# Performance work log

Measured on AMD Instinct MI355X. Metric: run time of the kernel, lower is better.

Reference implementation:

```python
import jax, jax.numpy as jnp
import numpy as np

B, N, D = 8, 4096, 256
H = 8
DH = D // H          # 32 per-head dim
M = 256              # number of random features
DEPTH = 4
HID = 4 * D          # mlp hidden
EPS = 1e-6


def layernorm(x, g, b):
    mu = jnp.mean(x, axis=-1, keepdims=True)
    var = jnp.mean(jnp.square(x - mu), axis=-1, keepdims=True)
    return (x - mu) * jax.lax.rsqrt(var + EPS) * g + b


def _phi(t, proj, is_query):
    # t: (B,H,N,DH), proj: (M,DH) -> (B,H,N,M) nonnegative softmax-kernel features
    nrm = DH ** -0.25
    td = t * nrm
    u = jnp.einsum('bhnd,md->bhnm', td, proj)
    diag = 0.5 * jnp.sum(td * td, axis=-1, keepdims=True)
    if is_query:
        mx = jnp.max(u, axis=-1, keepdims=True)
    else:
        mx = jnp.max(u, axis=(-2, -1), keepdims=True)
    return (jnp.exp(u - diag - mx) + 1e-4) / jnp.sqrt(jnp.asarray(M, t.dtype))


def performer_attn(h, Wqkv, Wproj, bproj, proj):
    # h: (B,N,D)
    qkv = h @ Wqkv                                   # (B,N,3D)
    q, k, v = jnp.split(qkv, 3, axis=-1)
    to_heads = lambda t: t.reshape(B, N, H, DH).transpose(0, 2, 1, 3)
    q, k, v = to_heads(q), to_heads(k), to_heads(v)  # (B,H,N,DH)
    qp = _phi(q, proj, True)                         # (B,H,N,M)
    kp = _phi(k, proj, False)                        # (B,H,N,M)
    kv = jnp.einsum('bhnm,bhnd->bhmd', kp, v)        # (B,H,M,DH) linear-time context
    z = 1.0 / (jnp.einsum('bhnm,bhm->bhn', qp, kp.sum(axis=2)) + 1e-6)
    out = jnp.einsum('bhnm,bhmd->bhnd', qp, kv) * z[..., None]
    out = out.transpose(0, 2, 1, 3).reshape(B, N, D)
    return out @ Wproj + bproj


def mlp(h, W1, b1, W2, b2):
    return jax.nn.gelu(h @ W1 + b1, approximate=False) @ W2 + b2


def setup_inputs() -> dict:
    key = jax.random.key(0)
    ks = jax.random.split(key, 10)
    inp = {
        'x': jax.random.normal(ks[0], (B, N, D), jnp.float32),
        'pos_emb': 0.02 * jax.random.normal(ks[1], (N, D), jnp.float32),
        'g1n': jnp.ones((D,), jnp.float32),
        'b1n': jnp.zeros((D,), jnp.float32),
        'g2n': jnp.ones((D,), jnp.float32),
        'b2n': jnp.zeros((D,), jnp.float32),
        'Wqkv': 0.02 * jax.random.normal(ks[2], (DEPTH, D, 3 * D), jnp.float32),
        'Wproj': 0.02 * jax.random.normal(ks[3], (DEPTH, D, D), jnp.float32),
        'bproj': jnp.zeros((DEPTH, D), jnp.float32),
        'W1': 0.02 * jax.random.normal(ks[4], (DEPTH, D, HID), jnp.float32),
        'b1m': jnp.zeros((DEPTH, HID), jnp.float32),
        'W2': 0.02 * jax.random.normal(ks[5], (DEPTH, HID, D), jnp.float32),
        'b2m': jnp.zeros((DEPTH, D), jnp.float32),
        'proj_mat': jax.random.normal(ks[6], (DEPTH, M, DH), jnp.float32),
    }
    return inp


def reference(x, pos_emb, g1n, b1n, g2n, b2n, Wqkv, Wproj, bproj, W1, b1m, W2, b2m, proj_mat):
    h = x + pos_emb[None]
    for l in range(DEPTH):  # small fixed depth
        h = h + performer_attn(layernorm(h, g1n, b1n), Wqkv[l], Wproj[l], bproj[l], proj_mat[l])
        h = h + mlp(layernorm(h, g2n, b2n), W1[l], b1m[l], W2[l], b2m[l])
    return h
```

## Files before the change

kernel.cpp:

```cpp
#include <hip/hip_runtime.h>
#include <hip/hip_bf16.h>
#include <math.h>

#define B 8
#define N 4096
#define D 256
#define H 8
#define DH 32
#define M 256
#define DEPTH 4
#define HID 1024
#define NRM 0.4204482076268573f

typedef __attribute__((ext_vector_type(8))) short short8;
typedef __attribute__((ext_vector_type(4))) float f32x4;

static __device__ __forceinline__ unsigned short f2bf(float f) {
    __hip_bfloat16 h = __float2bfloat16(f);
    return __builtin_bit_cast(unsigned short, h);
}
static __device__ __forceinline__ float bfu2f(unsigned short u) {
    unsigned int x = ((unsigned int)u) << 16;
    return __builtin_bit_cast(float, x);
}

__global__ void add_pos_kernel(const float* __restrict__ x, const float* __restrict__ pos,
                               float* __restrict__ h) {
    int i = blockIdx.x * 256 + threadIdx.x;
    int nd = i % (N * D);
    h[i] = x[i] + pos[nd];
}

__global__ void projbf_kernel(const float* __restrict__ in, unsigned short* __restrict__ out) {
    int i = blockIdx.x * 256 + threadIdx.x;
    out[i] = f2bf(in[i]);
}

__global__ __launch_bounds__(256) void wtrans_kernel(const float* __restrict__ in,
                                                     unsigned short* __restrict__ out,
                                                     int Kd, int Nd, int slim) {
    __shared__ float tl[32][33];
    int n0 = blockIdx.x * 32, k0 = blockIdx.y * 32;
    int t = threadIdx.x;
    int kk = t >> 3, c4 = (t & 7) * 4;
    float4 v = *reinterpret_cast<const float4*>(&in[(size_t)(k0 + kk) * Nd + n0 + c4]);
    tl[kk][c4 + 0] = v.x; tl[kk][c4 + 1] = v.y; tl[kk][c4 + 2] = v.z; tl[kk][c4 + 3] = v.w;
    __syncthreads();
    int nn = t >> 3, k4 = (t & 7) * 4;
    float sc = (n0 + nn < slim) ? NRM : 1.0f;
    ushort4 o;
    o.x = f2bf(tl[k4 + 0][nn] * sc); o.y = f2bf(tl[k4 + 1][nn] * sc);
    o.z = f2bf(tl[k4 + 2][nn] * sc); o.w = f2bf(tl[k4 + 3][nn] * sc);
    *reinterpret_cast<ushort4*>(&out[(size_t)(n0 + nn) * Kd + k0 + k4]) = o;
}

__global__ __launch_bounds__(256) void ln_kernel(const float* __restrict__ in,
                                                 const float* __restrict__ g,
                                                 const float* __restrict__ bb,
                                                 unsigned short* __restrict__ out) {
    int wave = threadIdx.x >> 6, lane = threadIdx.x & 63;
    long row = (long)blockIdx.x * 4 + wave;
    float4 v = reinterpret_cast<const float4*>(in + row * D)[lane];
    float s = v.x + v.y + v.z + v.w;
#pragma unroll
    for (int o = 32; o >= 1; o >>= 1) s += __shfl_xor(s, o);
    float mu = s * (1.0f / D);
    float d0 = v.x - mu, d1 = v.y - mu, d2 = v.z - mu, d3 = v.w - mu;
    float ss = d0 * d0 + d1 * d1 + d2 * d2 + d3 * d3;
#pragma unroll
    for (int o = 32; o >= 1; o >>= 1) ss += __shfl_xor(ss, o);
    float inv = rsqrtf(ss * (1.0f / D) + 1e-6f);
    float4 gv = reinterpret_cast<const float4*>(g)[lane];
    float4 bv = reinterpret_cast<const float4*>(bb)[lane];
    ushort4 o4;
    o4.x = f2bf(d0 * inv * gv.x + bv.x);
    o4.y = f2bf(d1 * inv * gv.y + bv.y);
    o4.z = f2bf(d2 * inv * gv.z + bv.z);
    o4.w = f2bf(d3 * inv * gv.w + bv.w);
    *reinterpret_cast<ushort4*>(&out[row * D + lane * 4]) = o4;
}

template <bool BIAS, bool GELU_ACT, bool RESID, bool OUT16>
__global__ __launch_bounds__(256) void mgemm_kernel(const unsigned short* __restrict__ A,
                                                    const unsigned short* __restrict__ Bt,
                                                    const float* __restrict__ bias,
                                                    float* __restrict__ C,
                                                    unsigned short* __restrict__ O16,
                                                    int K, int Nc) {
    __shared__ short Als[128][40];
    __shared__ short Bls[128][40];
    int t = threadIdx.x;
    int l = t & 63, w = t >> 6;
    int wr = w >> 1, wc = w & 1;
    int nwg = gridDim.x * gridDim.y;
    int bid = blockIdx.y * gridDim.x + blockIdx.x;
    int lgid = (bid & 7) * (nwg >> 3) + (bid >> 3);
    int bx = lgid % gridDim.x;
    int by = lgid / gridDim.x;
    long m0 = (long)by * 128;
    int n0 = bx * 128;
    int lr = l & 15;
    int lg = l >> 4;
    int kp8 = lg * 8;
    int srow = t >> 2, skoff = (t & 3) * 8;

    const unsigned short* Ap0 = &A[(size_t)(m0 + srow) * K + skoff];
    const unsigned short* Ap1 = Ap0 + (size_t)64 * K;
    const unsigned short* Bp0 = &Bt[(size_t)(n0 + srow) * K + skoff];
    const unsigned short* Bp1 = Bp0 + (size_t)64 * K;

    short8 ra0 = *reinterpret_cast<const short8*>(Ap0);
    short8 ra1 = *reinterpret_cast<const short8*>(Ap1);
    short8 rb0 = *reinterpret_cast<const short8*>(Bp0);
    short8 rb1 = *reinterpret_cast<const short8*>(Bp1);

    f32x4 acc[4][4];
#pragma unroll
    for (int i = 0; i < 4; i++)
#pragma unroll
        for (int j = 0; j < 4; j++) acc[i][j] = (f32x4){0.f, 0.f, 0.f, 0.f};

    for (int k0 = 0; k0 < K; k0 += 32) {
        *reinterpret_cast<short8*>(&Als[srow][skoff]) = ra0;
        *reinterpret_cast<short8*>(&Als[srow + 64][skoff]) = ra1;
        *reinterpret_cast<short8*>(&Bls[srow][skoff]) = rb0;
        *reinterpret_cast<short8*>(&Bls[srow + 64][skoff]) = rb1;
        __syncthreads();
        if (k0 + 32 < K) {
            ra0 = *reinterpret_cast<const short8*>(Ap0 + k0 + 32);
            ra1 = *reinterpret_cast<const short8*>(Ap1 + k0 + 32);
            rb0 = *reinterpret_cast<const short8*>(Bp0 + k0 + 32);
            rb1 = *reinterpret_cast<const short8*>(Bp1 + k0 + 32);
        }
        short8 a[4], b[4];
#pragma unroll
        for (int i = 0; i < 4; i++)
            a[i] = *reinterpret_cast<const short8*>(&Als[wr * 64 + i * 16 + lr][kp8]);
#pragma unroll
        for (int j = 0; j < 4; j++)
            b[j] = *reinterpret_cast<const short8*>(&Bls[wc * 64 + j * 16 + lr][kp8]);
#pragma unroll
        for (int i = 0; i < 4; i++)
#pragma unroll
            for (int j = 0; j < 4; j++)
                acc[i][j] = __builtin_amdgcn_mfma_f32_16x16x32_bf16(b[j], a[i], acc[i][j], 0, 0, 0);
        __syncthreads();
    }

    float4 bias4[4];
    if (BIAS) {
#pragma unroll
        for (int j = 0; j < 4; j++)
            bias4[j] = *reinterpret_cast<const float4*>(&bias[n0 + wc * 64 + j * 16 + lg * 4]);
    }
#pragma unroll
    for (int i = 0; i < 4; i++) {
        long grow = m0 + wr * 64 + i * 16 + lr;
#pragma unroll
        for (int j = 0; j < 4; j++) {
            int gcol = n0 + wc * 64 + j * 16 + lg * 4;
            f32x4 v = acc[i][j];
            if (BIAS) {
                v[0] += bias4[j].x; v[1] += bias4[j].y; v[2] += bias4[j].z; v[3] += bias4[j].w;
            }
            if (GELU_ACT) {
#pragma unroll
                for (int r = 0; r < 4; r++)
                    v[r] = 0.5f * v[r] * (1.0f + erff(v[r] * 0.70710678118654752f));
            }
            if (OUT16) {
                short4 o;
                o.x = (short)f2bf(v[0]); o.y = (short)f2bf(v[1]);
                o.z = (short)f2bf(v[2]); o.w = (short)f2bf(v[3]);
                *reinterpret_cast<short4*>(&O16[grow * Nc + gcol]) = o;
            } else if (RESID) {
                float4 c0 = *reinterpret_cast<const float4*>(&C[grow * Nc + gcol]);
                c0.x += v[0]; c0.y += v[1]; c0.z += v[2]; c0.w += v[3];
                *reinterpret_cast<float4*>(&C[grow * Nc + gcol]) = c0;
            } else {
                float4 c0 = {v[0], v[1], v[2], v[3]};
                *reinterpret_cast<float4*>(&C[grow * Nc + gcol]) = c0;
            }
        }
    }
}

#define KV_P 16
#define KV_ROWS (N / KV_P)
#define PSZ 8484
__global__ __launch_bounds__(256) void kv_kernel(const unsigned short* __restrict__ qkv16,
                                                 const unsigned short* __restrict__ projbf,
                                                 float* __restrict__ kvp) {
    __shared__ __align__(16) unsigned short kp_s[256][64];
    __shared__ __align__(16) unsigned short vT_s[32][66];
    __shared__ float red[4];
    __shared__ float asumred[4][256];
    __shared__ float vred[256][4];
    int t = threadIdx.x;
    int l = t & 63, w = t >> 6;
    int lr = l & 15, lg = l >> 4;
    int bh = blockIdx.x, b = bh >> 3, h = bh & 7;
    int n0 = blockIdx.y * KV_ROWS;
    int rsw = (lr & 7) << 3;

    f32x4 kvacc[4][2];
#pragma unroll
    for (int mf = 0; mf < 4; mf++)
#pragma unroll
        for (int dd = 0; dd < 2; dd++) kvacc[mf][dd] = (f32x4){0.f, 0.f, 0.f, 0.f};
    float asum_p[16];
#pragma unroll
    for (int f = 0; f < 16; f++) asum_p[f] = 0.f;
    float4 vs4 = {0.f, 0.f, 0.f, 0.f};
    float Lm = -1e30f;

    for (int c = 0; c < KV_ROWS / 64; c++) {
        size_t kbase = ((size_t)(b * N) + n0 + c * 64 + w * 16 + lr) * 768 + 256 + h * 32 + lg * 8;
        short8 aq = *reinterpret_cast<const short8*>(qkv16 + kbase);
        float sq = 0.f;
#pragma unroll
        for (int e = 0; e < 8; e++) {
            float xx = bfu2f((unsigned short)aq[e]);
            sq += xx * xx;
        }
        sq += __shfl_xor(sq, 16);
        sq += __shfl_xor(sq, 32);
        f32x4 ua[16];
#pragma unroll
        for (int f = 0; f < 16; f++) {
            short8 bq = *reinterpret_cast<const short8*>(projbf + (f * 16 + lr) * 32 + lg * 8);
            ua[f] = __builtin_amdgcn_mfma_f32_16x16x32_bf16(aq, bq, (f32x4){0.f, 0.f, 0.f, 0.f}, 0, 0, 0);
        }
        float cm = -1e30f;
#pragma unroll
        for (int f = 0; f < 16; f++)
#pragma unroll
            for (int r = 0; r < 4; r++) cm = fmaxf(cm, ua[f][r]);
#pragma unroll
        for (int o = 1; o < 64; o <<= 1) cm = fmaxf(cm, __shfl_xor(cm, o));
        if (l == 0) red[w] = cm;
        __syncthreads();
        float bm = fmaxf(fmaxf(red[0], red[1]), fmaxf(red[2], red[3]));
        if (bm > Lm) {
            float sc = __expf(Lm - bm);
#pragma unroll
            for (int mf = 0; mf < 4; mf++)
#pragma unroll
                for (int dd = 0; dd < 2; dd++) {
                    kvacc[mf][dd][0] *= sc; kvacc[mf][dd][1] *= sc;
                    kvacc[mf][dd][2] *= sc; kvacc[mf][dd][3] *= sc;
                }
#pragma unroll
            for (int f = 0; f < 16; f++) asum_p[f] *= sc;
            Lm = bm;
        }
        float dgr[4];
#pragma unroll
        for (int r = 0; r < 4; r++) dgr[r] = 0.5f * __shfl(sq, lg * 4 + r);
        int cbase = (w * 16 + lg * 4) ^ rsw;
#pragma unroll
        for (int f = 0; f < 16; f++) {
            float p0 = __expf(ua[f][0] - dgr[0] - Lm);
            float p1 = __expf(ua[f][1] - dgr[1] - Lm);
            float p2 = __expf(ua[f][2] - dgr[2] - Lm);
            float p3 = __expf(ua[f][3] - dgr[3] - Lm);
            asum_p[f] += p0 + p1 + p2 + p3;
            short4 o;
            o.x = (short)f2bf(p0); o.y = (short)f2bf(p1);
            o.z = (short)f2bf(p2); o.w = (short)f2bf(p3);
            *reinterpret_cast<short4*>(&kp_s[f * 16 + lr][cbase]) = o;
        }
#pragma unroll
        for (int ii = 0; ii < 2; ii++) {
            int idx = t + ii * 256;
            int nn = idx >> 3, dz = (idx & 7) * 4;
            const unsigned short* vp =
                qkv16 + ((size_t)(b * N) + n0 + c * 64 + nn) * 768 + 512 + h * 32 + dz;
            short4 vv = *reinterpret_cast<const short4*>(vp);
            float v0 = bfu2f((unsigned short)vv.x), v1 = bfu2f((unsigned short)vv.y);
            float v2 = bfu2f((unsigned short)vv.z), v3 = bfu2f((unsigned short)vv.w);
            vs4.x += v0; vs4.y += v1; vs4.z += v2; vs4.w += v3;
            vT_s[dz + 0][nn] = (unsigned short)vv.x; vT_s[dz + 1][nn] = (unsigned short)vv.y;
            vT_s[dz + 2][nn] = (unsigned short)vv.z; vT_s[dz + 3][nn] = (unsigned short)vv.w;
        }
        __syncthreads();
#pragma unroll
        for (int ks = 0; ks < 2; ks++) {
            short8 bv0 = *reinterpret_cast<const short8*>(&vT_s[lr][ks * 32 + lg * 8]);
            short8 bv1 = *reinterpret_cast<const short8*>(&vT_s[16 + lr][ks * 32 + lg * 8]);
#pragma unroll
            for (int mf = 0; mf < 4; mf++) {
                short8 am = *reinterpret_cast<const short8*>(
                    &kp_s[w * 64 + mf * 16 + lr][(ks * 32 + lg * 8) ^ rsw]);
                kvacc[mf][0] = __builtin_amdgcn_mfma_f32_16x16x32_bf16(am, bv0, kvacc[mf][0], 0, 0, 0);
                kvacc[mf][1] = __builtin_amdgcn_mfma_f32_16x16x32_bf16(am, bv1, kvacc[mf][1], 0, 0, 0);
            }
        }
    }
#pragma unroll
    for (int f = 0; f < 16; f++) {
        asum_p[f] += __shfl_xor(asum_p[f], 16);
        asum_p[f] += __shfl_xor(asum_p[f], 32);
    }
    if (l < 16) {
#pragma unroll
        for (int f = 0; f < 16; f++) asumred[w][f * 16 + l] = asum_p[f];
    }
    vred[t][0] = vs4.x; vred[t][1] = vs4.y; vred[t][2] = vs4.z; vred[t][3] = vs4.w;
    __syncthreads();
    size_t base = ((size_t)bh * KV_P + blockIdx.y) * PSZ;
#pragma unroll
    for (int mf = 0; mf < 4; mf++)
#pragma unroll
        for (int dd = 0; dd < 2; dd++)
#pragma unroll
            for (int r = 0; r < 4; r++) {
                int m = w * 64 + mf * 16 + lg * 4 + r;
                int d = dd * 16 + lr;
                kvp[base + m * 32 + d] = kvacc[mf][dd][r];
            }
    {
        float s = asumred[0][t] + asumred[1][t] + asumred[2][t] + asumred[3][t];
        kvp[base + 8192 + t] = s;
    }
    if (t < 32) {
        int f4g = t >> 2, cc = t & 3;
        float s = 0.f;
#pragma unroll
        for (int g = 0; g < 32; g++) s += vred[g * 8 + f4g][cc];
        kvp[base + 8448 + t] = s;
    }
    if (t == 0) kvp[base + 8480] = Lm;
}

__global__ __launch_bounds__(256) void kv_combine_kernel(const float* __restrict__ kvp,
                                                         unsigned short* __restrict__ kvTb,
                                                         float* __restrict__ ksumf) {
    __shared__ float vst[32];
    int t = threadIdx.x;
    int bh = blockIdx.x >> 2, mq = blockIdx.x & 3;
    size_t base0 = (size_t)bh * KV_P * PSZ;
    float Lp[KV_P];
    float gm = -1e30f;
#pragma unroll
    for (int p = 0; p < KV_P; p++) {
        Lp[p] = kvp[base0 + p * PSZ + 8480];
        gm = fmaxf(gm, Lp[p]);
    }
    if (t < 32) {
        float s = 0.f;
#pragma unroll
        for (int p = 0; p < KV_P; p++) s += kvp[base0 + p * PSZ + 8448 + t];
        vst[t] = s;
    }
    __syncthreads();
    int m = mq * 64 + (t >> 2);
    int d0 = (t & 3) * 8;
    float4 av0 = {0.f, 0.f, 0.f, 0.f}, av1 = {0.f, 0.f, 0.f, 0.f};
    float S = 0.f;
#pragma unroll
    for (int p = 0; p < KV_P; p++) {
        float e = __expf(Lp[p] - gm);
        size_t pb = base0 + p * PSZ;
        float4 a = *reinterpret_cast<const float4*>(&kvp[pb + m * 32 + d0]);
        float4 bq = *reinterpret_cast<const float4*>(&kvp[pb + m * 32 + d0 + 4]);
        av0.x += e * a.x; av0.y += e * a.y; av0.z += e * a.z; av0.w += e * a.w;
        av1.x += e * bq.x; av1.y += e * bq.y; av1.z += e * bq.z; av1.w += e * bq.w;
        if ((t & 3) == 0) S += e * kvp[pb + 8192 + m];
    }
    float o[8];
    o[0] = av0.x; o[1] = av0.y; o[2] = av0.z; o[3] = av0.w;
    o[4] = av1.x; o[5] = av1.y; o[6] = av1.z; o[7] = av1.w;
#pragma unroll
    for (int j = 0; j < 8; j++) {
        float v = (o[j] + 1e-4f * vst[d0 + j]) * 0.0625f;
        kvTb[((size_t)bh * 32 + d0 + j) * 256 + m] = f2bf(v);
    }
    if ((t & 3) == 0) ksumf[bh * 256 + m] = (S + 1e-4f * (float)N) * 0.0625f;
}

#define ATT_TILES 8
__global__ __launch_bounds__(256) void attn_kernel(const unsigned short* __restrict__ qkv16,
                                                   const unsigned short* __restrict__ projbf,
                                                   const unsigned short* __restrict__ kvTb,
                                                   const float* __restrict__ ksumf,
                                                   unsigned short* __restrict__ attn16) {
    __shared__ __align__(16) unsigned short qp_s[64 * 256];
    int t = threadIdx.x;
    int l = t & 63, w = t >> 6;
    int lr = l & 15, lg = l >> 4;
    int bh = blockIdx.x, b = bh >> 3, h = bh & 7;
    int swz = (lr & 7) << 3;
    int row = w * 16 + lr;

    const unsigned short* kvb = kvTb + (size_t)bh * 32 * 256;
    short8 kva0[8], kva1[8];
#pragma unroll
    for (int k0 = 0; k0 < 8; k0++) {
        kva0[k0] = *reinterpret_cast<const short8*>(kvb + (size_t)lr * 256 + k0 * 32 + lg * 8);
        kva1[k0] = *reinterpret_cast<const short8*>(kvb + (size_t)(16 + lr) * 256 + k0 * 32 + lg * 8);
    }

    int tile0 = blockIdx.y * ATT_TILES;
    size_t qstep = (size_t)64 * 768;
    size_t qbase = ((size_t)(b * N) + tile0 * 64 + w * 16 + lr) * 768 + h * 32 + lg * 8;
    short8 qf = *reinterpret_cast<const short8*>(qkv16 + qbase);

    for (int tl = 0; tl < ATT_TILES; tl++) {
        short8 qfn = qf;
        if (tl < ATT_TILES - 1)
            qfn = *reinterpret_cast<const short8*>(qkv16 + qbase + (size_t)(tl + 1) * qstep);

        float sq = 0.f;
#pragma unroll
        for (int e = 0; e < 8; e++) {
            float xx = bfu2f((unsigned short)qf[e]);
            sq += xx * xx;
        }
        sq += __shfl_xor(sq, 16);
        sq += __shfl_xor(sq, 32);
        float dg = 0.5f * sq;

        f32x4 ua[16];
#pragma unroll
        for (int f = 0; f < 16; f++) {
            short8 bq = *reinterpret_cast<const short8*>(projbf + (f * 16 + lr) * 32 + lg * 8);
            ua[f] = __builtin_amdgcn_mfma_f32_16x16x32_bf16(bq, qf, (f32x4){0.f, 0.f, 0.f, 0.f}, 0, 0, 0);
        }

        float mx = -1e30f;
#pragma unroll
        for (int f = 0; f < 16; f++)
#pragma unroll
            for (int r = 0; r < 4; r++) mx = fmaxf(mx, ua[f][r]);
        mx = fmaxf(mx, __shfl_xor(mx, 16));
        mx = fmaxf(mx, __shfl_xor(mx, 32));

        float zs = 0.f;
#pragma unroll
        for (int f = 0; f < 16; f++) {
            float4 ks4 = *reinterpret_cast<const float4*>(&ksumf[bh * 256 + f * 16 + lg * 4]);
            float p0 = (__expf(ua[f][0] - dg - mx) + 1e-4f) * 0.0625f;
            float p1 = (__expf(ua[f][1] - dg - mx) + 1e-4f) * 0.0625f;
            float p2 = (__expf(ua[f][2] - dg - mx) + 1e-4f) * 0.0625f;
            float p3 = (__expf(ua[f][3] - dg - mx) + 1e-4f) * 0.0625f;
            zs += p0 * ks4.x + p1 * ks4.y + p2 * ks4.z + p3 * ks4.w;
            short4 o;
            o.x = (short)f2bf(p0); o.y = (short)f2bf(p1);
            o.z = (short)f2bf(p2); o.w = (short)f2bf(p3);
            *reinterpret_cast<short4*>(&qp_s[row * 256 + ((f * 16 + lg * 4) ^ swz)]) = o;
        }
        zs += __shfl_xor(zs, 16);
        zs += __shfl_xor(zs, 32);
        float zf = 1.0f / (zs + 1e-6f);

        f32x4 oacc[2];
        oacc[0] = (f32x4){0.f, 0.f, 0.f, 0.f};
        oacc[1] = (f32x4){0.f, 0.f, 0.f, 0.f};
#pragma unroll
        for (int k0 = 0; k0 < 8; k0++) {
            short8 qpf = *reinterpret_cast<const short8*>(
                &qp_s[row * 256 + ((k0 * 32 + lg * 8) ^ swz)]);
            oacc[0] = __builtin_amdgcn_mfma_f32_16x16x32_bf16(kva0[k0], qpf, oacc[0], 0, 0, 0);
            oacc[1] = __builtin_amdgcn_mfma_f32_16x16x32_bf16(kva1[k0], qpf, oacc[1], 0, 0, 0);
        }
        size_t orow = ((size_t)(b * N) + (tile0 + tl) * 64 + w * 16 + lr) * 256 + h * 32;
#pragma unroll
        for (int dd = 0; dd < 2; dd++) {
            short4 o;
            o.x = (short)f2bf(oacc[dd][0] * zf);
            o.y = (short)f2bf(oacc[dd][1] * zf);
            o.z = (short)f2bf(oacc[dd][2] * zf);
            o.w = (short)f2bf(oacc[dd][3] * zf);
            *reinterpret_cast<short4*>(&attn16[orow + dd * 16 + lg * 4]) = o;
        }
        qf = qfn;
    }
}

extern "C" void kernel_launch(void* const* d_in, const int* in_sizes, int n_in,
                              void* d_out, int out_size, void* d_ws, size_t ws_size,
                              hipStream_t stream) {
    const float* x = (const float*)d_in[0];
    const float* pos = (const float*)d_in[1];
    const float* g1 = (const float*)d_in[2];
    const float* b1 = (const float*)d_in[3];
    const float* g2 = (const float*)d_in[4];
    const float* b2 = (const float*)d_in[5];
    const float* Wqkv = (const float*)d_in[6];
    const float* Wproj = (const float*)d_in[7];
    const float* bproj = (const float*)d_in[8];
    const float* W1 = (const float*)d_in[9];
    const float* b1m = (const float*)d_in[10];
    const float* W2 = (const float*)d_in[11];
    const float* b2m = (const float*)d_in[12];
    const float* projm = (const float*)d_in[13];

    float* h = (float*)d_out;
    char* p = (char*)d_ws;
    auto alloc = [&](size_t bytes) { char* r = p; p += (bytes + 255) & ~(size_t)255; return r; };
    unsigned short* wbf    = (unsigned short*)alloc((size_t)DEPTH * 786432 * 2);
    unsigned short* projb  = (unsigned short*)alloc((size_t)DEPTH * M * DH * 2);
    unsigned short* ln16   = (unsigned short*)alloc((size_t)B * N * D * 2);
    unsigned short* qkv16  = (unsigned short*)alloc((size_t)B * N * HID * 2);
    unsigned short* hid16  = qkv16;
    unsigned short* attn16 = (unsigned short*)alloc((size_t)B * N * D * 2);
    float* kvp             = (float*)alloc((size_t)64 * KV_P * PSZ * 4);
    unsigned short* kvTb   = (unsigned short*)alloc((size_t)64 * 32 * 256 * 2);
    float* ksumf           = (float*)alloc((size_t)64 * 256 * 4);

    for (int l = 0; l < DEPTH; l++) {
        size_t lb = (size_t)l * 786432;
        wtrans_kernel<<<dim3(768 / 32, 256 / 32), 256, 0, stream>>>(
            Wqkv + (size_t)l * D * 3 * D, wbf + lb + 0, 256, 768, 512);
        wtrans_kernel<<<dim3(256 / 32, 256 / 32), 256, 0, stream>>>(
            Wproj + (size_t)l * D * D, wbf + lb + 196608, 256, 256, 0);
        wtrans_kernel<<<dim3(1024 / 32, 256 / 32), 256, 0, stream>>>(
            W1 + (size_t)l * D * HID, wbf + lb + 262144, 256, 1024, 0);
        wtrans_kernel<<<dim3(256 / 32, 1024 / 32), 256, 0, stream>>>(
            W2 + (size_t)l * HID * D, wbf + lb + 524288, 1024, 256, 0);
    }
    projbf_kernel<<<DEPTH * M * DH / 256, 256, 0, stream>>>(projm, projb);

    add_pos_kernel<<<B * N * D / 256, 256, 0, stream>>>(x, pos, h);

    for (int l = 0; l < DEPTH; l++) {
        size_t lb = (size_t)l * 786432;
        const unsigned short* wqT = wbf + lb + 0;
        const unsigned short* wpT = wbf + lb + 196608;
        const unsigned short* w1T = wbf + lb + 262144;
        const unsigned short* w2T = wbf + lb + 524288;
        const float* bp = bproj + (size_t)l * D;
        const float* b1l = b1m + (size_t)l * HID;
        const float* b2l = b2m + (size_t)l * D;
        const unsigned short* prb = projb + (size_t)l * M * DH;

        ln_kernel<<<B * N / 4, 256, 0, stream>>>(h, g1, b1, ln16);
        mgemm_kernel<false, false, false, true><<<dim3(768 / 128, B * N / 128), 256, 0, stream>>>(
            ln16, wqT, nullptr, nullptr, qkv16, 256, 768);
        kv_kernel<<<dim3(B * H, KV_P), 256, 0, stream>>>(qkv16, prb, kvp);
        kv_combine_kernel<<<B * H * 4, 256, 0, stream>>>(kvp, kvTb, ksumf);
        attn_kernel<<<dim3(B * H, (N / 64) / ATT_TILES), 256, 0, stream>>>(
            qkv16, prb, kvTb, ksumf, attn16);
        mgemm_kernel<true, false, true, false><<<dim3(256 / 128, B * N / 128), 256, 0, stream>>>(
            attn16, wpT, bp, h, nullptr, 256, 256);
        ln_kernel<<<B * N / 4, 256, 0, stream>>>(h, g2, b2, ln16);
        mgemm_kernel<true, true, false, true><<<dim3(1024 / 128, B * N / 128), 256, 0, stream>>>(
            ln16, w1T, b1l, nullptr, hid16, 256, 1024);
        mgemm_kernel<true, false, true, false><<<dim3(256 / 128, B * N / 128), 256, 0, stream>>>(
            hid16, w2T, b2l, h, nullptr, 1024, 256);
    }
}
```

Baseline: 975.1 us.

## Drop online max rescaling in KV partials and transpose partial layout

The per-chunk block-wide max reduction, its barrier, and the rescaling of the KV accumulators are removed. Features are now exponentiated without subtracting a running max, and a single block max is taken at the end. The combine kernel then applies one exp(-gmax) factor instead of per-partition weights. The partial KV buffer is stored transposed (d-major) so that both the partial kernel's writes and the combine kernel's reads and bf16 writes become contiguous vector accesses. In exchange, the exponentials are no longer max-shifted, so very large projections could overflow fp32 or bf16 where the old form stayed bounded.

```diff
diff --git a/kernel.cpp b/kernel.cpp
--- a/kernel.cpp
+++ b/kernel.cpp
@@ -212,9 +212,10 @@
 #pragma unroll
     for (int f = 0; f < 16; f++) asum_p[f] = 0.f;
     float4 vs4 = {0.f, 0.f, 0.f, 0.f};
-    float Lm = -1e30f;
+    float cmax = -1e30f;
 
     for (int c = 0; c < KV_ROWS / 64; c++) {
+        __syncthreads();
         size_t kbase = ((size_t)(b * N) + n0 + c * 64 + w * 16 + lr) * 768 + 256 + h * 32 + lg * 8;
         short8 aq = *reinterpret_cast<const short8*>(qkv16 + kbase);
         float sq = 0.f;
@@ -225,45 +226,19 @@
         }
         sq += __shfl_xor(sq, 16);
         sq += __shfl_xor(sq, 32);
-        f32x4 ua[16];
+        float dgr[4];
+#pragma unroll
+        for (int r = 0; r < 4; r++) dgr[r] = 0.5f * __shfl(sq, lg * 4 + r);
+        int cbase = (w * 16 + lg * 4) ^ rsw;
 #pragma unroll
         for (int f = 0; f < 16; f++) {
             short8 bq = *reinterpret_cast<const short8*>(projbf + (f * 16 + lr) * 32 + lg * 8);
-            ua[f] = __builtin_amdgcn_mfma_f32_16x16x32_bf16(aq, bq, (f32x4){0.f, 0.f, 0.f, 0.f}, 0, 0, 0);
-        }
-        float cm = -1e30f;
-#pragma unroll
-        for (int f = 0; f < 16; f++)
-#pragma unroll
-            for (int r = 0; r < 4; r++) cm = fmaxf(cm, ua[f][r]);
-#pragma unroll
-        for (int o = 1; o < 64; o <<= 1) cm = fmaxf(cm, __shfl_xor(cm, o));
-        if (l == 0) red[w] = cm;
-        __syncthreads();
-        float bm = fmaxf(fmaxf(red[0], red[1]), fmaxf(red[2], red[3]));
-        if (bm > Lm) {
-            float sc = __expf(Lm - bm);
-#pragma unroll
-            for (int mf = 0; mf < 4; mf++)
-#pragma unroll
-                for (int dd = 0; dd < 2; dd++) {
-                    kvacc[mf][dd][0] *= sc; kvacc[mf][dd][1] *= sc;
-                    kvacc[mf][dd][2] *= sc; kvacc[mf][dd][3] *= sc;
-                }
-#pragma unroll
-            for (int f = 0; f < 16; f++) asum_p[f] *= sc;
-            Lm = bm;
-        }
-        float dgr[4];
-#pragma unroll
-        for (int r = 0; r < 4; r++) dgr[r] = 0.5f * __shfl(sq, lg * 4 + r);
-        int cbase = (w * 16 + lg * 4) ^ rsw;
-#pragma unroll
-        for (int f = 0; f < 16; f++) {
-            float p0 = __expf(ua[f][0] - dgr[0] - Lm);
-            float p1 = __expf(ua[f][1] - dgr[1] - Lm);
-            float p2 = __expf(ua[f][2] - dgr[2] - Lm);
-            float p3 = __expf(ua[f][3] - dgr[3] - Lm);
+            f32x4 u = __builtin_amdgcn_mfma_f32_16x16x32_bf16(aq, bq, (f32x4){0.f, 0.f, 0.f, 0.f}, 0, 0, 0);
+            cmax = fmaxf(cmax, fmaxf(fmaxf(u[0], u[1]), fmaxf(u[2], u[3])));
+            float p0 = __expf(u[0] - dgr[0]);
+            float p1 = __expf(u[1] - dgr[1]);
+            float p2 = __expf(u[2] - dgr[2]);
+            float p3 = __expf(u[3] - dgr[3]);
             asum_p[f] += p0 + p1 + p2 + p3;
             short4 o;
             o.x = (short)f2bf(p0); o.y = (short)f2bf(p1);
@@ -307,18 +282,22 @@
         for (int f = 0; f < 16; f++) asumred[w][f * 16 + l] = asum_p[f];
     }
     vred[t][0] = vs4.x; vred[t][1] = vs4.y; vred[t][2] = vs4.z; vred[t][3] = vs4.w;
+#pragma unroll
+    for (int o = 1; o < 64; o <<= 1) cmax = fmaxf(cmax, __shfl_xor(cmax, o));
+    if (l == 0) red[w] = cmax;
     __syncthreads();
     size_t base = ((size_t)bh * KV_P + blockIdx.y) * PSZ;
 #pragma unroll
     for (int mf = 0; mf < 4; mf++)
 #pragma unroll
-        for (int dd = 0; dd < 2; dd++)
-#pragma unroll
-            for (int r = 0; r < 4; r++) {
-                int m = w * 64 + mf * 16 + lg * 4 + r;
-                int d = dd * 16 + lr;
-                kvp[base + m * 32 + d] = kvacc[mf][dd][r];
-            }
+        for (int dd = 0; dd < 2; dd++) {
+            int m = w * 64 + mf * 16 + lg * 4;
+            int d = dd * 16 + lr;
+            float4 o;
+            o.x = kvacc[mf][dd][0]; o.y = kvacc[mf][dd][1];
+            o.z = kvacc[mf][dd][2]; o.w = kvacc[mf][dd][3];
+            *reinterpret_cast<float4*>(&kvp[base + (size_t)d * 256 + m]) = o;
+        }
     {
         float s = asumred[0][t] + asumred[1][t] + asumred[2][t] + asumred[3][t];
         kvp[base + 8192 + t] = s;
@@ -330,7 +309,7 @@
         for (int g = 0; g < 32; g++) s += vred[g * 8 + f4g][cc];
         kvp[base + 8448 + t] = s;
     }
-    if (t == 0) kvp[base + 8480] = Lm;
+    if (t == 0) kvp[base + 8480] = fmaxf(fmaxf(red[0], red[1]), fmaxf(red[2], red[3]));
 }
 
 __global__ __launch_bounds__(256) void kv_combine_kernel(const float* __restrict__ kvp,
@@ -338,15 +317,11 @@
                                                          float* __restrict__ ksumf) {
     __shared__ float vst[32];
     int t = threadIdx.x;
-    int bh = blockIdx.x >> 2, mq = blockIdx.x & 3;
+    int bh = blockIdx.x >> 2, dq = blockIdx.x & 3;
     size_t base0 = (size_t)bh * KV_P * PSZ;
-    float Lp[KV_P];
     float gm = -1e30f;
 #pragma unroll
-    for (int p = 0; p < KV_P; p++) {
-        Lp[p] = kvp[base0 + p * PSZ + 8480];
-        gm = fmaxf(gm, Lp[p]);
-    }
+    for (int p = 0; p < KV_P; p++) gm = fmaxf(gm, kvp[base0 + p * PSZ + 8480]);
     if (t < 32) {
         float s = 0.f;
 #pragma unroll
@@ -354,29 +329,32 @@
         vst[t] = s;
     }
     __syncthreads();
-    int m = mq * 64 + (t >> 2);
-    int d0 = (t & 3) * 8;
-    float4 av0 = {0.f, 0.f, 0.f, 0.f}, av1 = {0.f, 0.f, 0.f, 0.f};
-    float S = 0.f;
+    float es = __expf(-gm);
+    int d = dq * 8 + (t >> 5);
+    int m0 = (t & 31) * 8;
+    float4 a0 = {0.f, 0.f, 0.f, 0.f}, a1 = {0.f, 0.f, 0.f, 0.f};
 #pragma unroll
     for (int p = 0; p < KV_P; p++) {
-        float e = __expf(Lp[p] - gm);
-        size_t pb = base0 + p * PSZ;
-        float4 a = *reinterpret_cast<const float4*>(&kvp[pb + m * 32 + d0]);
-        float4 bq = *reinterpret_cast<const float4*>(&kvp[pb + m * 32 + d0 + 4]);
-        av0.x += e * a.x; av0.y += e * a.y; av0.z += e * a.z; av0.w += e * a.w;
-        av1.x += e * bq.x; av1.y += e * bq.y; av1.z += e * bq.z; av1.w += e * bq.w;
-        if ((t & 3) == 0) S += e * kvp[pb + 8192 + m];
-    }
-    float o[8];
-    o[0] = av0.x; o[1] = av0.y; o[2] = av0.z; o[3] = av0.w;
-    o[4] = av1.x; o[5] = av1.y; o[6] = av1.z; o[7] = av1.w;
-#pragma unroll
-    for (int j = 0; j < 8; j++) {
-        float v = (o[j] + 1e-4f * vst[d0 + j]) * 0.0625f;
-        kvTb[((size_t)bh * 32 + d0 + j) * 256 + m] = f2bf(v);
-    }
-    if ((t & 3) == 0) ksumf[bh * 256 + m] = (S + 1e-4f * (float)N) * 0.0625f;
+        const float* src = &kvp[base0 + p * PSZ + (size_t)d * 256 + m0];
+        float4 x0 = *reinterpret_cast<const float4*>(src);
+        float4 x1 = *reinterpret_cast<const float4*>(src + 4);
+        a0.x += x0.x; a0.y += x0.y; a0.z += x0.z; a0.w += x0.w;
+        a1.x += x1.x; a1.y += x1.y; a1.z += x1.z; a1.w += x1.w;
+    }
+    float vadd = 1e-4f * vst[d];
+    ushort4 o0, o1;
+    o0.x = f2bf((a0.x * es + vadd) * 0.0625f); o0.y = f2bf((a0.y * es + vadd) * 0.0625f);
+    o0.z = f2bf((a0.z * es + vadd) * 0.0625f); o0.w = f2bf((a0.w * es + vadd) * 0.0625f);
+    o1.x = f2bf((a1.x * es + vadd) * 0.0625f); o1.y = f2bf((a1.y * es + vadd) * 0.0625f);
+    o1.z = f2bf((a1.z * es + vadd) * 0.0625f); o1.w = f2bf((a1.w * es + vadd) * 0.0625f);
+    *reinterpret_cast<ushort4*>(&kvTb[((size_t)bh * 32 + d) * 256 + m0]) = o0;
+    *reinterpret_cast<ushort4*>(&kvTb[((size_t)bh * 32 + d) * 256 + m0 + 4]) = o1;
+    if (dq == 0) {
+        float S = 0.f;
+#pragma unroll
+        for (int p = 0; p < KV_P; p++) S += kvp[base0 + p * PSZ + 8192 + t];
+        ksumf[bh * 256 + t] = (S * es + 1e-4f * (float)N) * 0.0625f;
+    }
 }
 
 #define ATT_TILES 8
```

After: 913.3 us. -6.3%, faster.
